# Kernel optimization log

Measured on AMD Instinct MI355X. Metric: run time of the kernel, lower is better.

## Reference

```python
import jax, jax.numpy as jnp
import numpy as np

H = 16          # num_attention_heads
GRID = 16       # crop_size // patch_size
TOK_PER_FRAME = GRID * GRID


def _rope(x, pos, dim):
    # x: (B,H,N,dim), pos: (N,) int positions
    half = dim // 2
    omega = jnp.arange(half, dtype=x.dtype) / (dim / 2.0)
    inv = 1.0 / (10000.0 ** omega)                      # (half,)
    freq = pos.astype(x.dtype)[:, None] * inv            # (N, half)
    sin = jnp.concatenate([jnp.sin(freq), jnp.sin(freq)], axis=-1)  # (N, dim)  (tile, per source)
    cos = jnp.concatenate([jnp.cos(freq), jnp.cos(freq)], axis=-1)
    y = x.reshape(*x.shape[:-1], half, 2)
    y1, y2 = y[..., 0], y[..., 1]
    rot = jnp.stack((-y2, y1), axis=-1).reshape(x.shape)  # interleaved rotate-pairs
    return x * cos + rot * sin


def _apply_3d_rope(qk, f_ids, h_ids, w_ids, d_dim):
    s = 0
    parts = []
    for pos in (f_ids, h_ids, w_ids):
        parts.append(_rope(qk[..., s:s + d_dim], pos, d_dim))
        s += d_dim
    if s < qk.shape[-1]:
        parts.append(qk[..., s:])
    return jnp.concatenate(parts, axis=-1)


def setup_inputs() -> dict:
    key = jax.random.key(0)
    ks = jax.random.split(key, 5)
    D = 1024
    B, N = 4, 2048
    sc = 0.02
    return {
        "hidden_states": jax.random.normal(ks[0], (B, N, D), jnp.float32),
        "Wq": jax.random.normal(ks[1], (D, D), jnp.float32) * sc,
        "bq": jnp.zeros((D,), jnp.float32),
        "Wk": jax.random.normal(ks[2], (D, D), jnp.float32) * sc,
        "bk": jnp.zeros((D,), jnp.float32),
        "Wv": jax.random.normal(ks[3], (D, D), jnp.float32) * sc,
        "bv": jnp.zeros((D,), jnp.float32),
        "Wo": jax.random.normal(ks[4], (D, D), jnp.float32) * sc,
        "bo": jnp.zeros((D,), jnp.float32),
    }


def reference(hidden_states, Wq, bq, Wk, bk, Wv, bv, Wo, bo):
    B, N, D = hidden_states.shape
    hd = D // H
    d_dim = 2 * (hd // 3 // 2)  # per-component rotary dim (20 for hd=64)

    def heads(x):  # (B,N,D) -> (B,H,N,hd)
        return x.reshape(B, N, H, hd).transpose(0, 2, 1, 3)

    q = heads(hidden_states @ Wq + bq)
    k = heads(hidden_states @ Wk + bk)
    v = heads(hidden_states @ Wv + bv)

    ids = jnp.arange(N)
    f_ids = ids // TOK_PER_FRAME
    rem = ids - TOK_PER_FRAME * f_ids
    h_ids = rem // GRID
    w_ids = rem - GRID * h_ids

    q = _apply_3d_rope(q, f_ids, h_ids, w_ids, d_dim)
    k = _apply_3d_rope(k, f_ids, h_ids, w_ids, d_dim)

    scale = hd ** -0.5
    attn = jnp.einsum('bhqd,bhkd->bhqk', q, k) * scale
    attn = jax.nn.softmax(attn.astype(jnp.float32), axis=-1).astype(q.dtype)
    ctx = jnp.einsum('bhqk,bhkd->bhqd', attn, v)
    ctx = ctx.transpose(0, 2, 1, 3).reshape(B, N, D)
    return ctx @ Wo + bo
```

## Files before the change

### kernel.cpp

```cpp
#include <hip/hip_runtime.h>
#include <stdint.h>

#define H_   16
#define NS_  2048
#define B_   4
#define DM_  1024
#define HD_  64
#define MTOT (B_*NS_)

typedef __attribute__((ext_vector_type(8)))  short bf16x8;
typedef __attribute__((ext_vector_type(4)))  float f32x4;
typedef __attribute__((ext_vector_type(16))) float f32x16;

#define QSCALE 0.18033688011112042f

__device__ __forceinline__ unsigned short f2bf(float f){
  union { float f; unsigned u; } v; v.f = f;
  unsigned r = v.u + 0x7FFFu + ((v.u >> 16) & 1u);
  return (unsigned short)(r >> 16);
}
__device__ __forceinline__ float bf2f(unsigned short u){
  union { unsigned u; float f; } v; v.u = ((unsigned)u) << 16;
  return v.f;
}
__device__ __forceinline__ unsigned pk2(float a, float b){
  return (unsigned)f2bf(a) | ((unsigned)f2bf(b) << 16);
}
__device__ __forceinline__ unsigned cvtpk(float a, float b){
  unsigned r;
  asm("v_cvt_pk_bf16_f32 %0, %1, %2" : "=v"(r) : "v"(a), "v"(b));
  return r;
}
__device__ __forceinline__ float exp2a(float x){
  float r;
  asm("v_exp_f32 %0, %1" : "=v"(r) : "v"(x));
  return r;
}
__device__ __forceinline__ void gll16(const void* g, void* l){
  __builtin_amdgcn_global_load_lds(
      (const __attribute__((address_space(1))) unsigned int*)g,
      (__attribute__((address_space(3))) unsigned int*)l,
      16, 0, 0);
}

__global__ void k_prep(const float* __restrict__ hs, unsigned short* __restrict__ xb,
                       const float* __restrict__ W0, const float* __restrict__ W1,
                       const float* __restrict__ W2, const float* __restrict__ W3,
                       unsigned short* __restrict__ T0, unsigned short* __restrict__ T1,
                       unsigned short* __restrict__ T2, unsigned short* __restrict__ T3,
                       float2* __restrict__ tab)
{
  __shared__ float tile[64][65];
  const int bid = blockIdx.x, t = threadIdx.x;
  if (bid < 8192){
    long i = ((long)bid*256 + t)*4;
    float4 v = *(const float4*)(hs + i);
    ushort4 o; o.x=f2bf(v.x); o.y=f2bf(v.y); o.z=f2bf(v.z); o.w=f2bf(v.w);
    *(ushort4*)(xb + i) = o;
    return;
  }
  if (bid < 9216){
    int id = bid - 8192;
    const int z = id >> 8; id &= 255;
    const float* W = (z==0)? W0 : (z==1)? W1 : (z==2)? W2 : W3;
    unsigned short* Wt = (z==0)? T0 : (z==1)? T1 : (z==2)? T2 : T3;
    int kt = (id >> 4)*64, nt = (id & 15)*64;
    int r = t >> 4, c4 = (t & 15)*4;
#pragma unroll
    for (int i=0;i<4;i++){
      int k = r + i*16;
      float4 v = *(const float4*)(W + (size_t)(kt + k)*DM_ + nt + c4);
      tile[k][c4] = v.x; tile[k][c4+1]=v.y; tile[k][c4+2]=v.z; tile[k][c4+3]=v.w;
    }
    __syncthreads();
#pragma unroll
    for (int i=0;i<4;i++){
      int n = r + i*16;
      ushort4 o;
      o.x = f2bf(tile[c4+0][n]); o.y = f2bf(tile[c4+1][n]);
      o.z = f2bf(tile[c4+2][n]); o.w = f2bf(tile[c4+3][n]);
      *(ushort4*)(Wt + (size_t)(nt + n)*DM_ + kt + c4) = o;
    }
    return;
  }
  {
    int n = (bid - 9216)*256 + t;
    int f = n >> 8, rem = n & 255, hh = rem >> 4, ww = rem & 15;
    float pos[3]; pos[0]=(float)f; pos[1]=(float)hh; pos[2]=(float)ww;
#pragma unroll
    for (int c=0;c<3;c++)
#pragma unroll
      for (int i=0;i<10;i++){
        float inv = exp2f(-(float)i * 1.3287712379549449f);
        float s, co;
        sincosf(pos[c]*inv, &s, &co);
        tab[n*30 + c*10 + i] = make_float2(co, s);
      }
  }
}

__device__ __forceinline__ void stage128(const unsigned short* __restrict__ gsrc,
                                         char* ldst, int tid){
  const int srow = tid >> 3;
  const int gch  = (tid & 7) ^ (srow & 7);
  const unsigned short* gp = gsrc + (size_t)srow*DM_ + gch*8;
  char* lp = ldst + tid*16;
#pragma unroll
  for (int j=0;j<4;j++)
    gll16(gp + (size_t)(j*32)*DM_, lp + j*4096);
}

template<int MODE>
__global__ __launch_bounds__(256, 2) void k_gemm256(
    const unsigned short* __restrict__ A,
    const unsigned short* __restrict__ w0,
    const unsigned short* __restrict__ w1,
    const unsigned short* __restrict__ w2,
    const float* __restrict__ b0,
    const float* __restrict__ b1,
    const float* __restrict__ b2,
    unsigned short* __restrict__ Qb,
    unsigned short* __restrict__ Kb,
    unsigned short* __restrict__ VTb,
    float* __restrict__ Fout,
    const float2* __restrict__ tab)
{
  extern __shared__ char smem[];
  char* aL = smem;
  char* bL = smem + 32768;
  const int tid = threadIdx.x, lane = tid & 63, w = tid >> 6;
  const int qc = lane & 15, g = lane >> 4;
  const int wm = (w >> 1)*64, wn = (w & 1)*64;

  int mat, mt, nt;
  {
    int id = blockIdx.x;
    if (MODE == 0){
      int wg = (id & 7)*192 + (id >> 3);
      mat = wg >> 9; int rem = wg & 511;
      mt = (rem >> 3)*128; nt = (rem & 7)*128;
    } else {
      int wg = (id & 7)*64 + (id >> 3);
      mat = 0; mt = (wg >> 3)*128; nt = (wg & 7)*128;
    }
  }
  const unsigned short* Wt = (MODE==1)? w0 : ((mat==0)? w0 : (mat==1)? w1 : w2);
  const float* bias        = (MODE==1)? b0 : ((mat==0)? b0 : (mat==1)? b1 : b2);

  const unsigned short* Ab = A  + (size_t)mt*DM_;
  const unsigned short* Bb = Wt + (size_t)nt*DM_;

  stage128(Ab,      aL,         tid);
  stage128(Bb,      bL,         tid);
  stage128(Ab + 64, aL + 16384, tid);
  stage128(Bb + 64, bL + 16384, tid);

  f32x4 acc[4][4] = {};

  for (int kt = 0; kt < 16; ++kt){
    const int bu = kt & 1;
    if (kt < 15) asm volatile("s_waitcnt vmcnt(8)" ::: "memory");
    else         asm volatile("s_waitcnt vmcnt(0)" ::: "memory");
    __builtin_amdgcn_s_barrier();
    __builtin_amdgcn_sched_barrier(0);
    const char* aT = aL + bu*16384;
    const char* bT = bL + bu*16384;

    bf16x8 bfr[4][2], af[4][2];
#pragma unroll
    for (int n=0;n<4;n++)
#pragma unroll
      for (int ks=0;ks<2;ks++){
        int row = wn + n*16 + qc;
        bfr[n][ks] = *(const bf16x8*)(bT + row*128 + ((ks*64 + g*16) ^ ((row&7)<<4)));
      }
#pragma unroll
    for (int m=0;m<4;m++)
#pragma unroll
      for (int ks=0;ks<2;ks++){
        int row = wm + m*16 + qc;
        af[m][ks] = *(const bf16x8*)(aT + row*128 + ((ks*64 + g*16) ^ ((row&7)<<4)));
      }
    __builtin_amdgcn_s_setprio(1);
#pragma unroll
    for (int m=0;m<2;m++)
#pragma unroll
      for (int n=0;n<4;n++)
#pragma unroll
        for (int ks=0;ks<2;ks++)
          acc[m][n] = __builtin_amdgcn_mfma_f32_16x16x32_bf16(af[m][ks], bfr[n][ks], acc[m][n], 0,0,0);
    __builtin_amdgcn_s_setprio(0);
    asm volatile("s_waitcnt lgkmcnt(0)" ::: "memory");
    __builtin_amdgcn_sched_barrier(0);
    __builtin_amdgcn_s_barrier();
    __builtin_amdgcn_sched_barrier(0);
    if (kt < 14){
      stage128(Ab + (size_t)(kt+2)*64, aL + bu*16384, tid);
      stage128(Bb + (size_t)(kt+2)*64, bL + bu*16384, tid);
    }
    __builtin_amdgcn_s_setprio(1);
#pragma unroll
    for (int m=2;m<4;m++)
#pragma unroll
      for (int n=0;n<4;n++)
#pragma unroll
        for (int ks=0;ks<2;ks++)
          acc[m][n] = __builtin_amdgcn_mfma_f32_16x16x32_bf16(af[m][ks], bfr[n][ks], acc[m][n], 0,0,0);
    __builtin_amdgcn_s_setprio(0);
  }

  if (MODE == 1){
#pragma unroll
    for (int n=0;n<4;n++){
      int col = nt + wn + n*16 + qc;
      float bv = bias[col];
#pragma unroll
      for (int m=0;m<4;m++){
#pragma unroll
        for (int r=0;r<4;r++){
          int mrow = mt + wm + m*16 + g*4 + r;
          Fout[(size_t)mrow*DM_ + col] = acc[m][n][r] + bv;
        }
      }
    }
  } else if (mat < 2){
    unsigned short* out = (mat==0)? Qb : Kb;
    const float qsc = (mat==0)? QSCALE : 1.f;
#pragma unroll
    for (int n=0;n<4;n++){
      int col = nt + wn + n*16 + qc;
      float bv = bias[col];
      int d = col & 63;
      int c = d/20; int cm = (c > 2) ? 2 : c;
      int er = d - 20*cm; if (er >= 10) er -= 10;
      const bool rot  = (d < 60);
      const bool oddp = (d & 1);
      const float2* tbase = tab + (cm*10 + er);
#pragma unroll
      for (int m=0;m<4;m++){
#pragma unroll
        for (int r=0;r<4;r++){
          int mrow = mt + wm + m*16 + g*4 + r;
          int ntk = mrow & (NS_-1);
          float x = acc[m][n][r] + bv;
          float xp = __shfl_xor(x, 1);
          float2 cs = tbase[ntk*30];
          float y = rot ? (oddp ? (x*cs.x + xp*cs.y) : (x*cs.x - xp*cs.y)) : x;
          out[(size_t)mrow*DM_ + col] = f2bf(y * qsc);
        }
      }
    }
  } else {
#pragma unroll
    for (int n=0;n<4;n++){
      int col = nt + wn + n*16 + qc;
      float bv = bias[col];
      int hh = col >> 6, d = col & 63;
#pragma unroll
      for (int m=0;m<4;m++){
        int mrow0 = mt + wm + m*16 + g*4;
        int b = mrow0 >> 11, ntk = mrow0 & (NS_-1);
        int pos = (ntk & ~12) | ((ntk & 4) << 1) | ((ntk & 8) >> 1);
        ushort4 o;
        o.x = f2bf(acc[m][n][0] + bv);
        o.y = f2bf(acc[m][n][1] + bv);
        o.z = f2bf(acc[m][n][2] + bv);
        o.w = f2bf(acc[m][n][3] + bv);
        *(ushort4*)(VTb + (((size_t)(b*H_ + hh)*HD_ + d)*NS_ + pos)) = o;
      }
    }
  }
}

__global__ __launch_bounds__(256, 4) void k_attn(const unsigned short* __restrict__ Q,
                                                 const unsigned short* __restrict__ K,
                                                 const unsigned short* __restrict__ VT,
                                                 unsigned short* __restrict__ ctxout)
{
  __shared__ __attribute__((aligned(16))) char smem[32768];
  const int tid  = threadIdx.x;
  const int lane = tid & 63, w = tid >> 6;
  const int qcol = lane & 31, h = lane >> 5;
  const int sw   = (lane & 7) << 4;
  const int bh   = blockIdx.x;
  const int b    = bh >> 4, head = bh & 15;
  const int q0   = blockIdx.y*128 + w*32;

  const unsigned short* Qp = Q  + ((size_t)(b*NS_ + q0))*DM_ + head*HD_;
  const unsigned short* Kp = K  + ((size_t)(b*NS_))*DM_ + head*HD_;
  const unsigned short* Vp = VT + (size_t)bh*HD_*NS_;

  const int trow = tid >> 3;
  const int tc   = (tid & 7) ^ (trow & 7);

  bf16x8 qf[4];
#pragma unroll
  for (int i=0;i<4;i++)
    qf[i] = *(const bf16x8*)(Qp + (size_t)qcol*DM_ + 16*i + 8*h);

  bf16x8 ones;
#pragma unroll
  for (int i=0;i<8;i++) ones[i] = (short)0x3F80;

  {
    const unsigned short* gk = Kp + (size_t)trow*DM_ + tc*8;
    const unsigned short* gv = Vp + (size_t)trow*NS_ + tc*8;
    gll16(gk,          smem + w*1024);
    gll16(gk + 32*DM_, smem + 4096 + w*1024);
    gll16(gv,          smem + 8192 + w*1024);
    gll16(gv + 32*NS_, smem + 8192 + 4096 + w*1024);
  }

  f32x16 ctx0 = {}, ctx1 = {}, lacc = {};

  for (int t = 0; t < NS_/64; ++t){
    const int curo = (t & 1) * 16384;
    __syncthreads();
    if (t + 1 < NS_/64){
      const int kb = (t+1)*64;
      const int nxt = ((t+1) & 1) * 16384;
      const unsigned short* gk = Kp + (size_t)(kb + trow)*DM_ + tc*8;
      const unsigned short* gv = Vp + (size_t)trow*NS_ + kb + tc*8;
      gll16(gk,          smem + nxt + w*1024);
      gll16(gk + 32*DM_, smem + nxt + 4096 + w*1024);
      gll16(gv,          smem + nxt + 8192 + w*1024);
      gll16(gv + 32*NS_, smem + nxt + 8192 + 4096 + w*1024);
    }
    const char* kls = smem + curo;
    const char* vls = smem + curo + 8192;

    f32x16 st0 = {}, st1 = {};
    __builtin_amdgcn_s_setprio(1);
#pragma unroll
    for (int i=0;i<4;i++){
      bf16x8 kf = *(const bf16x8*)(kls + (((qcol)*128 + 32*i + 16*h) ^ sw));
      st0 = __builtin_amdgcn_mfma_f32_32x32x16_bf16(kf, qf[i], st0, 0,0,0);
    }
#pragma unroll
    for (int i=0;i<4;i++){
      bf16x8 kf = *(const bf16x8*)(kls + ((((32 + qcol)*128) + 32*i + 16*h) ^ sw));
      st1 = __builtin_amdgcn_mfma_f32_32x32x16_bf16(kf, qf[i], st1, 0,0,0);
    }
    __builtin_amdgcn_s_setprio(0);

    unsigned ua[8], ub[8];
#pragma unroll
    for (int r=0;r<8;r++)
      ua[r] = cvtpk(exp2a(st0[2*r]), exp2a(st0[2*r+1]));
#pragma unroll
    for (int r=0;r<8;r++)
      ub[r] = cvtpk(exp2a(st1[2*r]), exp2a(st1[2*r+1]));
    bf16x8 pfA0 = __builtin_bit_cast(bf16x8, make_uint4(ua[0],ua[1],ua[2],ua[3]));
    bf16x8 pfA1 = __builtin_bit_cast(bf16x8, make_uint4(ua[4],ua[5],ua[6],ua[7]));
    bf16x8 pfB0 = __builtin_bit_cast(bf16x8, make_uint4(ub[0],ub[1],ub[2],ub[3]));
    bf16x8 pfB1 = __builtin_bit_cast(bf16x8, make_uint4(ub[4],ub[5],ub[6],ub[7]));

    __builtin_amdgcn_s_setprio(1);
    lacc = __builtin_amdgcn_mfma_f32_32x32x16_bf16(ones, pfA0, lacc, 0,0,0);
    lacc = __builtin_amdgcn_mfma_f32_32x32x16_bf16(ones, pfA1, lacc, 0,0,0);
    lacc = __builtin_amdgcn_mfma_f32_32x32x16_bf16(ones, pfB0, lacc, 0,0,0);
    lacc = __builtin_amdgcn_mfma_f32_32x32x16_bf16(ones, pfB1, lacc, 0,0,0);
#pragma unroll
    for (int s=0; s<2; ++s){
#pragma unroll
      for (int kc=0; kc<2; ++kc){
        const bf16x8 pf = s ? (kc ? pfB1 : pfB0) : (kc ? pfA1 : pfA0);
        bf16x8 vf0 = *(const bf16x8*)(vls + ((qcol)*128      + ((64*s + 32*kc + 16*h) ^ sw)));
        ctx0 = __builtin_amdgcn_mfma_f32_32x32x16_bf16(vf0, pf, ctx0, 0,0,0);
        bf16x8 vf1 = *(const bf16x8*)(vls + ((32 + qcol)*128 + ((64*s + 32*kc + 16*h) ^ sw)));
        ctx1 = __builtin_amdgcn_mfma_f32_32x32x16_bf16(vf1, pf, ctx1, 0,0,0);
      }
    }
    __builtin_amdgcn_s_setprio(0);
  }

  float linv = 1.f / lacc[0];
  __syncthreads();
  char* reg = smem + w*4096;
#pragma unroll
  for (int rq=0; rq<4; ++rq){
    int db0 = 8*rq + 4*h;
    uint2 v0, v1;
    v0.x = pk2(ctx0[4*rq+0]*linv, ctx0[4*rq+1]*linv);
    v0.y = pk2(ctx0[4*rq+2]*linv, ctx0[4*rq+3]*linv);
    v1.x = pk2(ctx1[4*rq+0]*linv, ctx1[4*rq+1]*linv);
    v1.y = pk2(ctx1[4*rq+2]*linv, ctx1[4*rq+3]*linv);
    *(uint2*)(reg + qcol*128 + db0*2)      = v0;
    *(uint2*)(reg + qcol*128 + (32+db0)*2) = v1;
  }
  __syncthreads();
  unsigned short* outp = ctxout + ((size_t)(b*NS_ + q0))*DM_ + head*HD_;
#pragma unroll
  for (int p=0;p<4;p++){
    int row = p*8 + (lane>>3);
    uint4 v = *(const uint4*)(reg + row*128 + (lane&7)*16);
    *(uint4*)(outp + (size_t)row*DM_ + (lane&7)*8) = v;
  }
}

extern "C" void kernel_launch(void* const* d_in, const int* in_sizes, int n_in,
                              void* d_out, int out_size, void* d_ws, size_t ws_size,
                              hipStream_t stream)
{
  const float* hs = (const float*)d_in[0];
  const float* Wq = (const float*)d_in[1];
  const float* bq = (const float*)d_in[2];
  const float* Wk = (const float*)d_in[3];
  const float* bk = (const float*)d_in[4];
  const float* Wv = (const float*)d_in[5];
  const float* bv = (const float*)d_in[6];
  const float* Wo = (const float*)d_in[7];
  const float* bo = (const float*)d_in[8];

  char* ws = (char*)d_ws;
  size_t off = 0;
  auto alloc = [&](size_t b){ void* p = ws + off; off += (b + 255) & ~(size_t)255; return p; };
  unsigned short* xb  = (unsigned short*)alloc((size_t)MTOT*DM_*2);
  unsigned short* wqt = (unsigned short*)alloc((size_t)DM_*DM_*2);
  unsigned short* wkt = (unsigned short*)alloc((size_t)DM_*DM_*2);
  unsigned short* wvt = (unsigned short*)alloc((size_t)DM_*DM_*2);
  unsigned short* wot = (unsigned short*)alloc((size_t)DM_*DM_*2);
  float2*         tab = (float2*)alloc((size_t)NS_*30*sizeof(float2));
  unsigned short* Qb  = (unsigned short*)alloc((size_t)MTOT*DM_*2);
  unsigned short* Kb  = (unsigned short*)alloc((size_t)MTOT*DM_*2);
  unsigned short* VTb = (unsigned short*)alloc((size_t)MTOT*DM_*2);
  unsigned short* cxb = (unsigned short*)alloc((size_t)MTOT*DM_*2);

  hipFuncSetAttribute((const void*)k_gemm256<0>,
                      hipFuncAttributeMaxDynamicSharedMemorySize, 65536);
  hipFuncSetAttribute((const void*)k_gemm256<1>,
                      hipFuncAttributeMaxDynamicSharedMemorySize, 65536);

  k_prep<<<dim3(9224), dim3(256), 0, stream>>>(hs, xb, Wq, Wk, Wv, Wo,
                                               wqt, wkt, wvt, wot, tab);

  k_gemm256<0><<<dim3(1536), dim3(256), 65536, stream>>>(
      xb, wqt, wkt, wvt, bq, bk, bv, Qb, Kb, VTb, (float*)nullptr, tab);

  k_attn<<<dim3(64, 16), dim3(256), 0, stream>>>(Qb, Kb, VTb, cxb);

  k_gemm256<1><<<dim3(512), dim3(256), 65536, stream>>>(
      cxb, wot, nullptr, nullptr, bo, nullptr, nullptr,
      nullptr, nullptr, nullptr, (float*)d_out, nullptr);
}
```

Before: 199.1 us.

## Triple-buffer K tiles and prefetch two steps ahead in attention kernel

Restructures the attention kernel's K/V staging so K uses three LDS buffers and is prefetched two iterations ahead, while V stays double-buffered one ahead. It replaces __syncthreads with an explicit partial vmcnt wait plus s_barrier, so the loads still in flight do not stall the loop. The goal is to hide more global-load latency behind the MFMA work. In exchange, LDS per block grows from 32 KB to 40 KB, which may lower occupancy, and correctness now depends on the manual waitcnt bookkeeping.

```diff
diff --git a/kernel.cpp b/kernel.cpp
--- a/kernel.cpp
+++ b/kernel.cpp
@@ -277,7 +277,7 @@
                                                  const unsigned short* __restrict__ VT,
                                                  unsigned short* __restrict__ ctxout)
 {
-  __shared__ __attribute__((aligned(16))) char smem[32768];
+  __shared__ __attribute__((aligned(16))) char smem[40960];
   const int tid  = threadIdx.x;
   const int lane = tid & 63, w = tid >> 6;
   const int qcol = lane & 31, h = lane >> 5;
@@ -302,32 +302,34 @@
 #pragma unroll
   for (int i=0;i<8;i++) ones[i] = (short)0x3F80;
 
-  {
-    const unsigned short* gk = Kp + (size_t)trow*DM_ + tc*8;
-    const unsigned short* gv = Vp + (size_t)trow*NS_ + tc*8;
-    gll16(gk,          smem + w*1024);
-    gll16(gk + 32*DM_, smem + 4096 + w*1024);
-    gll16(gv,          smem + 8192 + w*1024);
-    gll16(gv + 32*NS_, smem + 8192 + 4096 + w*1024);
-  }
+  const unsigned short* gkb = Kp + (size_t)trow*DM_ + tc*8;
+  const unsigned short* gvb = Vp + (size_t)trow*NS_ + tc*8;
+#define STAGE_K(t_, ki_) { char* d = smem + (ki_)*8192 + w*1024;                 \
+    gll16(gkb + (size_t)(t_)*64*DM_, d);                                         \
+    gll16(gkb + (size_t)((t_)*64 + 32)*DM_, d + 4096); }
+#define STAGE_V(t_) { char* d = smem + 24576 + ((t_)&1)*8192 + w*1024;           \
+    gll16(gvb + (t_)*64, d);                                                     \
+    gll16(gvb + 32*NS_ + (t_)*64, d + 4096); }
+
+  STAGE_K(0, 0);
+  STAGE_V(0);
+  STAGE_K(1, 1);
 
   f32x16 ctx0 = {}, ctx1 = {}, lacc = {};
-
-  for (int t = 0; t < NS_/64; ++t){
-    const int curo = (t & 1) * 16384;
-    __syncthreads();
-    if (t + 1 < NS_/64){
-      const int kb = (t+1)*64;
-      const int nxt = ((t+1) & 1) * 16384;
-      const unsigned short* gk = Kp + (size_t)(kb + trow)*DM_ + tc*8;
-      const unsigned short* gv = Vp + (size_t)trow*NS_ + kb + tc*8;
-      gll16(gk,          smem + nxt + w*1024);
-      gll16(gk + 32*DM_, smem + nxt + 4096 + w*1024);
-      gll16(gv,          smem + nxt + 8192 + w*1024);
-      gll16(gv + 32*NS_, smem + nxt + 8192 + 4096 + w*1024);
-    }
-    const char* kls = smem + curo;
-    const char* vls = smem + curo + 8192;
+  int ki = 0;
+
+  for (int t = 0; t < 32; ++t){
+    if (t < 31) asm volatile("s_waitcnt vmcnt(2)" ::: "memory");
+    else        asm volatile("s_waitcnt vmcnt(0)" ::: "memory");
+    __builtin_amdgcn_s_barrier();
+    __builtin_amdgcn_sched_barrier(0);
+    if (t < 31) STAGE_V(t+1);
+    if (t < 30){
+      int kn = ki + 2; if (kn >= 3) kn -= 3;
+      STAGE_K(t+2, kn);
+    }
+    const char* kls = smem + ki*8192;
+    const char* vls = smem + 24576 + (t&1)*8192;
 
     f32x16 st0 = {}, st1 = {};
     __builtin_amdgcn_s_setprio(1);
@@ -372,7 +374,11 @@
       }
     }
     __builtin_amdgcn_s_setprio(0);
-  }
+
+    ki = (ki + 1 == 3) ? 0 : ki + 1;
+  }
+#undef STAGE_K
+#undef STAGE_V
 
   float linv = 1.f / lacc[0];
   __syncthreads();
```

Result: no change. 200.2 us (+0.6%).
